# Kernel tuning notes

Measured on AMD Instinct MI355X. Metric: run time of the kernel, lower is better.

## Reference

```python
import jax, jax.numpy as jnp
import numpy as np

B, F, H, D, S = 32, 512, 8, 64, 256
TOPK = max(1, int(0.1 * F))  # 51
BETA0 = 0.6


def setup_inputs() -> dict:
    key = jax.random.key(0)
    k1, k2, k3 = jax.random.split(key, 3)
    values = jax.random.normal(k1, (B, F, H, D), jnp.float32)
    data_logits = jax.random.normal(k2, (B, F, H, S), jnp.float32)
    # alpha is orthogonal-initialized in torch; normal init preserves the math being tested
    alpha = jax.random.normal(k3, (H, S, F), jnp.float32)
    inv_softplus = np.float32(BETA0 + np.log1p(-np.exp(-BETA0)))
    beta_param = jnp.full((H, S, 1), inv_softplus, jnp.float32)
    return {"values": values, "data_logits": data_logits, "alpha": alpha, "beta_param": beta_param}


def _topk_mask(logits, k):
    # keep exactly top-k per row (last axis), others -> -inf (matches torch topk+scatter)
    topv, topi = jax.lax.top_k(logits, k)            # [..., k]
    shp = logits.shape
    n = int(np.prod(shp[:-1]))
    flat = jnp.full((n, shp[-1]), -jnp.inf, logits.dtype)
    rows = jnp.arange(n)[:, None]
    flat = flat.at[rows, topi.reshape(n, k)].set(topv.reshape(n, k))
    return flat.reshape(shp)


def reference(values, data_logits, alpha, beta_param):
    scale = 1.0 / np.sqrt(alpha.shape[-1])
    alpha_logits = alpha * scale                       # [H,S,F]
    dl = jnp.transpose(data_logits, (0, 2, 3, 1))      # [B,H,S,F]
    mu = dl.mean(axis=-1, keepdims=True)
    std = jnp.sqrt(dl.var(axis=-1, keepdims=True) + 1e-6) + 1e-6
    dl = (dl - mu) / std
    beta_eff = jax.nn.softplus(beta_param)             # [H,S,1]
    logits = alpha_logits[None] + beta_eff[None] * dl  # [B,H,S,F]
    logits = _topk_mask(logits, TOPK)
    attn = jax.nn.softmax(logits, axis=-1)             # dropout omitted (eval mode)
    out = jnp.einsum('bhsf,bfhd->bshd', attn, values)  # [B,S,H,D]
    return out
```

## Files before the change

### kernel.cpp

```cpp
#include <hip/hip_runtime.h>
#include <hip/hip_bf16.h>
#include <stdint.h>
#include <math.h>

#define NB 32
#define NF 512
#define NH 8
#define ND 64
#define NS 256
#define TOPK 51
#define STILE 16
#define LDSF (NF + 1)

__device__ __forceinline__ float wave_sum_f32(float v) {
#pragma unroll
  for (int o = 32; o > 0; o >>= 1) v += __shfl_xor(v, o, 64);
  return v;
}

__device__ __forceinline__ float np_pairwise_sum_512(const float* __restrict__ row, int lane) {
  const int c2 = lane & 31;
  const int k  = c2 >> 3;
  const int c  = c2 & 7;
  const float* blk = row + 128 * k;
  float r = blk[c];
#pragma unroll
  for (int m = 1; m < 16; ++m) r += blk[c + 8 * m];
  float s = r + __shfl_xor(r, 1, 64);
  s = s + __shfl_xor(s, 2, 64);
  s = s + __shfl_xor(s, 4, 64);
  float u = s + __shfl_xor(s, 8, 64);
  u = u + __shfl_xor(u, 16, 64);
  return u;
}

__global__ __launch_bounds__(1024, 8)
void gating_attention_kernel(const float* __restrict__ vals,
                             const float* __restrict__ dlg,
                             const float* __restrict__ alpha,
                             const float* __restrict__ betap,
                             float* __restrict__ out)
{
#pragma clang fp contract(off)
  __shared__ float dl_t[STILE * LDSF];
  __shared__ uint2 pairs[STILE][64];

  const int blk  = blockIdx.x;
  const int bh   = blk >> 4;
  const int t    = blk & 15;
  const int b    = bh >> 3;
  const int h    = bh & 7;
  const int s0   = t * STILE;
  const int tid  = threadIdx.x;
  const int w    = tid >> 6;
  const int lane = tid & 63;
  const unsigned long long lmask = (1ull << lane) - 1ull;
  const float scalef = (float)0.04419417382415922;

#pragma unroll
  for (int cc = 0; cc < 2; ++cc) {
    int i  = cc * 1024 + tid;
    int f  = i >> 2;
    int sg = (i & 3) << 2;
    const float4 v4 = *reinterpret_cast<const float4*>(
        dlg + ((((size_t)b * NF + f) * NH + h) * NS + (size_t)(s0 + sg)));
    dl_t[(sg + 0) * LDSF + f] = v4.x;
    dl_t[(sg + 1) * LDSF + f] = v4.y;
    dl_t[(sg + 2) * LDSF + f] = v4.z;
    dl_t[(sg + 3) * LDSF + f] = v4.w;
  }
  __syncthreads();

  const int s = s0 + w;
  float* row = dl_t + w * LDSF;

  float a[8], x[8];
#pragma unroll
  for (int j = 0; j < 8; ++j)
    a[j] = alpha[((size_t)h * NS + s) * NF + lane + 64 * j];
#pragma unroll
  for (int j = 0; j < 8; ++j)
    x[j] = row[lane + 64 * j];

  const float S1 = np_pairwise_sum_512(row, lane);
  const float mu = S1 * (1.0f / 512.0f);

  float tv[8];
#pragma unroll
  for (int j = 0; j < 8; ++j) {
    tv[j] = x[j] - mu;
    row[lane + 64 * j] = tv[j] * tv[j];
  }
  const float S2  = np_pairwise_sum_512(row, lane);
  const float var = S2 * (1.0f / 512.0f);
  const float stdv = (float)sqrt((double)(var + 1e-6f)) + 1e-6f;

  const float bp = betap[h * NS + s];
  const float eb = (float)exp((double)bp);
  const float beta = (float)log1p((double)eb);

  float lg[8];
  unsigned key[8];
#pragma unroll
  for (int j = 0; j < 8; ++j) {
    float z  = tv[j] / stdv;
    float m  = beta * z;
    float af = a[j] * scalef;
    float l  = af + m;
    lg[j] = l;
    unsigned bits = __float_as_uint(l);
    key[j] = (bits & 0x80000000u) ? ~bits : (bits | 0x80000000u);
  }

  unsigned kmax = key[0], kmin = key[0];
#pragma unroll
  for (int j = 1; j < 8; ++j) {
    kmax = key[j] > kmax ? key[j] : kmax;
    kmin = key[j] < kmin ? key[j] : kmin;
  }
#pragma unroll
  for (int o = 32; o > 0; o >>= 1) {
    unsigned om = (unsigned)__shfl_xor((int)kmax, o, 64);
    unsigned on = (unsigned)__shfl_xor((int)kmin, o, 64);
    kmax = om > kmax ? om : kmax;
    kmin = on < kmin ? on : kmin;
  }

  unsigned lo = kmin, hi = kmax;
  int cnt = NF;
  while (lo < hi) {
    unsigned mid = hi - ((hi - lo) >> 1);
    int cm = 0;
#pragma unroll
    for (int j = 0; j < 8; ++j) cm += __popcll(__ballot(key[j] >= mid));
    if (cm >= TOPK) { lo = mid; cnt = cm; if (cm == TOPK) break; }
    else hi = mid - 1;
  }
  const unsigned T = lo;
  const bool exact = (cnt == TOPK);

  bool keep[8];
  if (exact) {
#pragma unroll
    for (int j = 0; j < 8; ++j) keep[j] = (key[j] >= T);
  } else {
    int g = 0;
#pragma unroll
    for (int j = 0; j < 8; ++j) g += __popcll(__ballot(key[j] > T));
    const int need = TOPK - g;
    int cumt = 0;
#pragma unroll
    for (int j = 0; j < 8; ++j) {
      unsigned long long meq = __ballot(key[j] == T);
      int tr = cumt + __popcll(meq & lmask);
      cumt += __popcll(meq);
      keep[j] = (key[j] > T) || ((key[j] == T) && (tr < need));
    }
  }

  unsigned tb = (T & 0x80000000u) ? (T ^ 0x80000000u) : ~T;
  const float thrf = __uint_as_float(tb);

  float p[8];
  float zs = 0.0f;
#pragma unroll
  for (int j = 0; j < 8; ++j) {
    float e = keep[j] ? __expf(lg[j] - thrf) : 0.0f;
    p[j] = e;
    zs += e;
  }
  zs = wave_sum_f32(zs);
  const float rz = 1.0f / zs;

  int base = 0;
#pragma unroll
  for (int j = 0; j < 8; ++j) {
    unsigned long long mk = __ballot(keep[j]);
    int idx = base + __popcll(mk & lmask);
    if (keep[j]) pairs[w][idx] = make_uint2((unsigned)(lane + 64 * j), __float_as_uint(p[j]));
    base += __popcll(mk);
  }
  const int nk = (TOPK + 3) & ~3;
  if (lane >= TOPK && lane < nk) pairs[w][lane] = make_uint2(0u, 0u);

  const float* vb = vals + (((size_t)b * NF) * NH + h) * ND + lane;
  float acc0 = 0.0f, acc1 = 0.0f, acc2 = 0.0f, acc3 = 0.0f;
  for (int k0 = 0; k0 < nk; k0 += 4) {
    uint2 e0 = pairs[w][k0 + 0];
    uint2 e1 = pairs[w][k0 + 1];
    uint2 e2 = pairs[w][k0 + 2];
    uint2 e3 = pairs[w][k0 + 3];
    float v0 = vb[e0.x * (NH * ND)];
    float v1 = vb[e1.x * (NH * ND)];
    float v2 = vb[e2.x * (NH * ND)];
    float v3 = vb[e3.x * (NH * ND)];
    acc0 = fmaf(__uint_as_float(e0.y), v0, acc0);
    acc1 = fmaf(__uint_as_float(e1.y), v1, acc1);
    acc2 = fmaf(__uint_as_float(e2.y), v2, acc2);
    acc3 = fmaf(__uint_as_float(e3.y), v3, acc3);
  }
  const float acc = (acc0 + acc1) + (acc2 + acc3);

  out[(((size_t)b * NS + s) * NH + h) * ND + lane] = acc * rz;
}

extern "C" void kernel_launch(void* const* d_in, const int* in_sizes, int n_in,
                              void* d_out, int out_size, void* d_ws, size_t ws_size,
                              hipStream_t stream) {
  const float* vals  = (const float*)d_in[0];
  const float* dlg   = (const float*)d_in[1];
  const float* alpha = (const float*)d_in[2];
  const float* betap = (const float*)d_in[3];
  float* out = (float*)d_out;

  dim3 grid(NB * NH * (NS / STILE));
  dim3 block(1024);
  gating_attention_kernel<<<grid, block, 0, stream>>>(vals, dlg, alpha, betap, out);
}
```

Baseline: 129.6 us.

## Pad LDS rows, precompute softplus beta, reorder blocks, and trim per-element math

```diff
diff --git a/kernel.cpp b/kernel.cpp
--- a/kernel.cpp
+++ b/kernel.cpp
@@ -10,19 +10,24 @@
 #define NS 256
 #define TOPK 51
 #define STILE 16
-#define LDSF (NF + 1)
+#define LDSF 537
 
 __device__ __forceinline__ float wave_sum_f32(float v) {
 #pragma unroll
   for (int o = 32; o > 0; o >>= 1) v += __shfl_xor(v, o, 64);
   return v;
+}
+
+__device__ __forceinline__ int lane_prefix(unsigned long long m) {
+  return __builtin_amdgcn_mbcnt_hi((unsigned)(m >> 32),
+         __builtin_amdgcn_mbcnt_lo((unsigned)m, 0u));
 }
 
 __device__ __forceinline__ float np_pairwise_sum_512(const float* __restrict__ row, int lane) {
   const int c2 = lane & 31;
   const int k  = c2 >> 3;
   const int c  = c2 & 7;
-  const float* blk = row + 128 * k;
+  const float* blk = row + 136 * k;
   float r = blk[c];
 #pragma unroll
   for (int m = 1; m < 16; ++m) r += blk[c + 8 * m];
@@ -34,11 +39,20 @@
   return u;
 }
 
+__global__ void beta_kernel(const float* __restrict__ bp, float* __restrict__ bf) {
+  int i = blockIdx.x * 1024 + threadIdx.x;
+  if (i < NH * NS) {
+    double e = exp((double)bp[i]);
+    bf[i] = (float)log1p(e);
+  }
+}
+
 __global__ __launch_bounds__(1024, 8)
 void gating_attention_kernel(const float* __restrict__ vals,
                              const float* __restrict__ dlg,
                              const float* __restrict__ alpha,
                              const float* __restrict__ betap,
+                             const float* __restrict__ betaf,
                              float* __restrict__ out)
 {
 #pragma clang fp contract(off)
@@ -46,15 +60,14 @@
   __shared__ uint2 pairs[STILE][64];
 
   const int blk  = blockIdx.x;
-  const int bh   = blk >> 4;
-  const int t    = blk & 15;
+  const int bh   = blk & 255;
+  const int t    = blk >> 8;
   const int b    = bh >> 3;
   const int h    = bh & 7;
   const int s0   = t * STILE;
   const int tid  = threadIdx.x;
   const int w    = tid >> 6;
   const int lane = tid & 63;
-  const unsigned long long lmask = (1ull << lane) - 1ull;
   const float scalef = (float)0.04419417382415922;
 
 #pragma unroll
@@ -62,12 +75,13 @@
     int i  = cc * 1024 + tid;
     int f  = i >> 2;
     int sg = (i & 3) << 2;
+    int fo = f + ((f >> 7) << 3);
     const float4 v4 = *reinterpret_cast<const float4*>(
         dlg + ((((size_t)b * NF + f) * NH + h) * NS + (size_t)(s0 + sg)));
-    dl_t[(sg + 0) * LDSF + f] = v4.x;
-    dl_t[(sg + 1) * LDSF + f] = v4.y;
-    dl_t[(sg + 2) * LDSF + f] = v4.z;
-    dl_t[(sg + 3) * LDSF + f] = v4.w;
+    dl_t[(sg + 0) * LDSF + fo] = v4.x;
+    dl_t[(sg + 1) * LDSF + fo] = v4.y;
+    dl_t[(sg + 2) * LDSF + fo] = v4.z;
+    dl_t[(sg + 3) * LDSF + fo] = v4.w;
   }
   __syncthreads();
 
@@ -80,7 +94,7 @@
     a[j] = alpha[((size_t)h * NS + s) * NF + lane + 64 * j];
 #pragma unroll
   for (int j = 0; j < 8; ++j)
-    x[j] = row[lane + 64 * j];
+    x[j] = row[lane + 64 * j + 8 * (j >> 1)];
 
   const float S1 = np_pairwise_sum_512(row, lane);
   const float mu = S1 * (1.0f / 512.0f);
@@ -89,21 +103,25 @@
 #pragma unroll
   for (int j = 0; j < 8; ++j) {
     tv[j] = x[j] - mu;
-    row[lane + 64 * j] = tv[j] * tv[j];
+    row[lane + 64 * j + 8 * (j >> 1)] = tv[j] * tv[j];
   }
   const float S2  = np_pairwise_sum_512(row, lane);
   const float var = S2 * (1.0f / 512.0f);
-  const float stdv = (float)sqrt((double)(var + 1e-6f)) + 1e-6f;
-
-  const float bp = betap[h * NS + s];
-  const float eb = (float)exp((double)bp);
-  const float beta = (float)log1p((double)eb);
-
+  const float stdv = sqrtf(var + 1e-6f) + 1e-6f;
+
+  float beta;
+  if (betaf) beta = betaf[h * NS + s];
+  else {
+    double e = exp((double)betap[h * NS + s]);
+    beta = (float)log1p(e);
+  }
+
+  const double rd = 1.0 / (double)stdv;
   float lg[8];
   unsigned key[8];
 #pragma unroll
   for (int j = 0; j < 8; ++j) {
-    float z  = tv[j] / stdv;
+    float z  = (float)((double)tv[j] * rd);
     float m  = beta * z;
     float af = a[j] * scalef;
     float l  = af + m;
@@ -152,7 +170,7 @@
 #pragma unroll
     for (int j = 0; j < 8; ++j) {
       unsigned long long meq = __ballot(key[j] == T);
-      int tr = cumt + __popcll(meq & lmask);
+      int tr = cumt + lane_prefix(meq);
       cumt += __popcll(meq);
       keep[j] = (key[j] > T) || ((key[j] == T) && (tr < need));
     }
@@ -176,8 +194,10 @@
 #pragma unroll
   for (int j = 0; j < 8; ++j) {
     unsigned long long mk = __ballot(keep[j]);
-    int idx = base + __popcll(mk & lmask);
-    if (keep[j]) pairs[w][idx] = make_uint2((unsigned)(lane + 64 * j), __float_as_uint(p[j]));
+    int idx = base + lane_prefix(mk);
+    if (keep[j])
+      pairs[w][idx] = make_uint2((unsigned)((lane + 64 * j) << 9),
+                                 __float_as_uint(p[j]));
     base += __popcll(mk);
   }
   const int nk = (TOPK + 3) & ~3;
@@ -190,10 +210,10 @@
     uint2 e1 = pairs[w][k0 + 1];
     uint2 e2 = pairs[w][k0 + 2];
     uint2 e3 = pairs[w][k0 + 3];
-    float v0 = vb[e0.x * (NH * ND)];
-    float v1 = vb[e1.x * (NH * ND)];
-    float v2 = vb[e2.x * (NH * ND)];
-    float v3 = vb[e3.x * (NH * ND)];
+    float v0 = vb[e0.x];
+    float v1 = vb[e1.x];
+    float v2 = vb[e2.x];
+    float v3 = vb[e3.x];
     acc0 = fmaf(__uint_as_float(e0.y), v0, acc0);
     acc1 = fmaf(__uint_as_float(e1.y), v1, acc1);
     acc2 = fmaf(__uint_as_float(e2.y), v2, acc2);
@@ -213,7 +233,13 @@
   const float* betap = (const float*)d_in[3];
   float* out = (float*)d_out;
 
+  float* betaf = nullptr;
+  if (ws_size >= (size_t)(NH * NS) * sizeof(float)) {
+    betaf = (float*)d_ws;
+    beta_kernel<<<2, 1024, 0, stream>>>(betap, betaf);
+  }
+
   dim3 grid(NB * NH * (NS / STILE));
   dim3 block(1024);
-  gating_attention_kernel<<<grid, block, 0, stream>>>(vals, dlg, alpha, betap, out);
-}
+  gating_attention_kernel<<<grid, block, 0, stream>>>(vals, dlg, alpha, betap, betaf, out);
+}
```

After: 117.7 us. 1.1x faster.
